# Kernel optimization log

Hardware: AMD Instinct MI355X
Metric: run time of the kernel (lower is better)

Reference implementation:

```python
import jax, jax.numpy as jnp
import numpy as np

D = 128      # d_feat / d_model
L = 512      # seq_len
H = 8        # heads (hardcoded in FourierBlock weights)
E = D // H   # head dim = 16
MODES = 64   # low-frequency modes (mode_select='low' -> index = range(MODES))
MA = 25      # moving_avg kernel
NL = 2       # e_layers
DFF = 512
EPS = 1e-5


def _positional(length, dim):
    pos = jnp.arange(length, dtype=jnp.float32)[:, None]
    div = jnp.exp(jnp.arange(0, dim, 2, dtype=jnp.float32) * (-np.log(10000.0) / dim))
    pe = jnp.zeros((length, dim), dtype=jnp.float32)
    pe = pe.at[:, 0::2].set(jnp.sin(pos * div))
    pe = pe.at[:, 1::2].set(jnp.cos(pos * div))
    return pe


def _mov_mean(x, k):
    # series_decomp moving average: replicate-pad (k-1)//2 each side, window mean stride 1
    pad = (k - 1) // 2
    xp = jnp.concatenate([jnp.repeat(x[:, :1], pad, axis=1), x,
                          jnp.repeat(x[:, -1:], pad, axis=1)], axis=1)
    cs = jnp.cumsum(xp, axis=1)
    cs = jnp.concatenate([jnp.zeros_like(cs[:, :1]), cs], axis=1)
    return (cs[:, k:] - cs[:, :-k]) / k


def _fourier_layer(x, Wq, bq, Wo, bo, fwr, fwi):
    # AutoCorrelationLayer(query proj -> FourierBlock -> out proj); k/v projections are unused by FourierBlock
    B = x.shape[0]
    q = (x @ Wq + bq).reshape(B, L, H, E).transpose(0, 2, 3, 1)   # B,H,E,L
    xft = jnp.fft.rfft(q, axis=-1)                                # B,H,E,L//2+1
    Wc = fwr + 1j * fwi                                           # H,E,E,M (complex mode weights)
    sel = jnp.einsum('bhem,heom->bhom', xft[..., :MODES], Wc)
    out_ft = jnp.zeros((B, H, E, L // 2 + 1), dtype=sel.dtype).at[..., :MODES].set(sel)
    y = jnp.fft.irfft(out_ft, n=L, axis=-1)                       # B,H,E,L
    y = y.reshape(B, L, H * E)  # matches torch .view(B, L, -1) on contiguous B,H,E,L
    return y @ Wo + bo


def _enc_layer(x, Wq, bq, Wo, bo, fwr, fwi, W1, W2):
    x = x + _fourier_layer(x, Wq, bq, Wo, bo, fwr, fwi)
    x = x - _mov_mean(x, MA)                                  # decomp1 seasonal part
    y = jax.nn.gelu(x @ W1, approximate=False) @ W2           # 1x1 convs == matmuls, no bias
    s = x + y
    return s - _mov_mean(s, MA)                               # decomp2 seasonal part


def setup_inputs() -> dict:
    key = jax.random.key(0)
    ks = jax.random.split(key, 12)
    B = 128
    scale = 1.0 / (D * D)
    return {
        "x_enc": jax.random.normal(ks[0], (B, D * L), dtype=jnp.float32),
        "x_mark_enc": jax.random.uniform(ks[1], (B, D * L), dtype=jnp.float32),
        "x_dec": jnp.zeros((1,), jnp.float32),
        "x_mark_dec": jnp.zeros((1,), jnp.float32),
        "conv_w": jax.random.normal(ks[2], (D, D, 3), dtype=jnp.float32) * 0.02,
        "Wq": jax.random.normal(ks[3], (NL, D, D), dtype=jnp.float32) * 0.02,
        "bq": jnp.zeros((NL, D), jnp.float32),
        "Wo": jax.random.normal(ks[4], (NL, D, D), dtype=jnp.float32) * 0.02,
        "bo": jnp.zeros((NL, D), jnp.float32),
        "fwr": jax.random.uniform(ks[5], (NL, H, E, E, MODES), dtype=jnp.float32) * scale,
        "fwi": jax.random.uniform(ks[6], (NL, H, E, E, MODES), dtype=jnp.float32) * scale,
        "W1": jax.random.normal(ks[7], (NL, D, DFF), dtype=jnp.float32) * 0.02,
        "W2": jax.random.normal(ks[8], (NL, DFF, D), dtype=jnp.float32) * 0.02,
        "ln_g": jnp.ones((D,), jnp.float32),
        "ln_b": jnp.zeros((D,), jnp.float32),
        "proj_w": jax.random.normal(ks[9], (D * L,), dtype=jnp.float32) * 0.002,
        "proj_b": jnp.zeros((), jnp.float32),
    }


def reference(x_enc, x_mark_enc, x_dec, x_mark_dec, conv_w, Wq, bq, Wo, bo,
              fwr, fwi, W1, W2, ln_g, ln_b, proj_w, proj_b):
    B = x_enc.shape[0]
    x = x_enc.reshape(B, D, L).transpose(0, 2, 1)          # B,L,D
    mark = x_mark_enc.reshape(B, D, L).transpose(0, 2, 1)  # B,L,D
    # TokenEmbedding: Conv1d kernel 3, circular padding, no bias
    xc = x.transpose(0, 2, 1)                              # B,D,L
    xp = jnp.concatenate([xc[:, :, -1:], xc, xc[:, :, :1]], axis=-1)
    tok = jax.lax.conv_general_dilated(xp, conv_w, (1,), 'VALID',
                                       dimension_numbers=('NCH', 'OIH', 'NCH'))
    h = tok.transpose(0, 2, 1) + _positional(L, D)[None]   # + sinusoidal PE (dropout=0)
    for l in range(NL):
        h = _enc_layer(h, Wq[l], bq[l], Wo[l], bo[l], fwr[l], fwi[l], W1[l], W2[l])
    # my_Layernorm: LayerNorm over features, then subtract mean over time axis
    mu = h.mean(-1, keepdims=True)
    var = h.var(-1, keepdims=True)
    hn = (h - mu) / jnp.sqrt(var + EPS) * ln_g + ln_b
    hn = hn - hn.mean(axis=1, keepdims=True)
    o = jax.nn.gelu(hn, approximate=False) * mark          # act + mask-mul
    return o.reshape(B, -1) @ proj_w + proj_b              # (B,) after squeeze
```

## Files before the change

### kernel.cpp

```cpp
#include <hip/hip_runtime.h>
#include <math.h>

#define DFF 512
#define NLAYER 2
#define TS_LD 132
#define CS_LD 130

typedef __bf16 bf16x8 __attribute__((ext_vector_type(8)));
typedef __bf16 bf16x4 __attribute__((ext_vector_type(4)));
typedef float f32x4 __attribute__((ext_vector_type(4)));

__device__ __forceinline__ float4 f4_load(const float* p) { return *(const float4*)p; }
__device__ __forceinline__ void f4_store(float* p, float4 v) { *(float4*)p = v; }
__device__ __forceinline__ float4 f4_zero() { return make_float4(0.f, 0.f, 0.f, 0.f); }
__device__ __forceinline__ float gelu_f(float x) {
    return 0.5f * x * (1.0f + erff(x * 0.70710678118654752440f));
}
__device__ __forceinline__ float gelu_fast(float x) {
    float z = 1.5957691216f * (x + 0.044715f * x * x * x);
    float e = __expf(z);
    return x - x / (e + 1.0f);
}
__device__ __forceinline__ void store_bf4(__bf16* p, float4 v) {
    __bf16 t[4] = {(__bf16)v.x, (__bf16)v.y, (__bf16)v.z, (__bf16)v.w};
    *(uint2*)p = *(uint2*)t;
}
__device__ __forceinline__ bf16x8 ld_b64x2(const __bf16* p) {
    bf16x4 lo = *(const bf16x4*)p;
    bf16x4 hi = *(const bf16x4*)(p + 4);
    return __builtin_shufflevector(lo, hi, 0, 1, 2, 3, 4, 5, 6, 7);
}

__global__ __launch_bounds__(256) void k_init(float* __restrict__ pe,
                                              __bf16* __restrict__ Fttb,
                                              __bf16* __restrict__ Gtb) {
    int idx = blockIdx.x * 256 + threadIdx.x;
    {
        int l = idx >> 7, d = idx & 127;
        int j = d >> 1;
        double div = exp((double)(2 * j) * (-log(10000.0) / 128.0));
        double a = (double)l * div;
        pe[idx] = (d & 1) ? (float)cos(a) : (float)sin(a);
    }
    {
        int m2 = idx >> 9, t = idx & 511;
        int m = m2 >> 1;
        int r = (m * t) & 511;
        double ang = (double)r * (6.283185307179586476925287 / 512.0);
        float cv = (float)cos(ang), sv = (float)sin(ang);
        float f = (m2 & 1) ? -sv : cv;
        Fttb[idx] = (__bf16)f;
        float s = (m == 0) ? (1.0f / 512.0f) : (2.0f / 512.0f);
        Gtb[t * 128 + m2] = (__bf16)(f * s);
    }
}

__global__ __launch_bounds__(256) void k_castw(const float* __restrict__ Wq,
                                               const float* __restrict__ Wo,
                                               const float* __restrict__ W1,
                                               const float* __restrict__ W2,
                                               const float* __restrict__ cw,
                                               __bf16* __restrict__ wbf,
                                               __bf16* __restrict__ cwtk) {
    int i = blockIdx.x * 256 + threadIdx.x;
    if (i < 65536) {
        int r = i & 16383, l = (i >> 14) & 1;
        int n = r >> 7, k = r & 127;
        const float* W = (i >= 32768) ? Wo : Wq;
        wbf[i] = (__bf16)W[l * 16384 + k * 128 + n];
    } else if (i < 196608) {
        int j = i - 65536;
        int l = j >> 16, r = j & 65535;
        int f = r >> 7, k = r & 127;
        wbf[i] = (__bf16)W1[l * 65536 + k * 512 + f];
    } else if (i < 327680) {
        int j = i - 196608;
        int l = j >> 16, r = j & 65535;
        int n = r >> 9, f = r & 511;
        wbf[i] = (__bf16)W2[l * 65536 + f * 128 + n];
    } else if (i < 376832) {
        int j = i - 327680;
        int s = j >> 14, r = j & 16383;
        int d = r >> 7, ii = r & 127;
        cwtk[j] = (__bf16)cw[(d * 128 + ii) * 3 + s];
    }
}

__global__ __launch_bounds__(256) void k_xpose(const float* __restrict__ xe,
                                               __bf16* __restrict__ xt) {
    __shared__ float ts[128][65];
    const int b = blockIdx.y, l0 = blockIdx.x * 64;
    for (int idx = threadIdx.x; idx < 128 * 16; idx += 256) {
        int d = idx >> 4, c4 = idx & 15;
        float4 v = f4_load(&xe[((size_t)b * 128 + d) * 512 + l0 + c4 * 4]);
        ts[d][c4 * 4 + 0] = v.x; ts[d][c4 * 4 + 1] = v.y;
        ts[d][c4 * 4 + 2] = v.z; ts[d][c4 * 4 + 3] = v.w;
    }
    __syncthreads();
#pragma unroll
    for (int p = 0; p < 4; ++p) {
        int l = (threadIdx.x >> 4) + p * 16;
        int d0 = (threadIdx.x & 15) * 8;
        __bf16 tmp[8];
#pragma unroll
        for (int j = 0; j < 8; ++j) tmp[j] = (__bf16)ts[d0 + j][l];
        *(uint4*)&xt[((size_t)b * 512 + l0 + l) * 128 + d0] = *(uint4*)tmp;
    }
}

__global__ __launch_bounds__(256, 4) void k_embed_m(const __bf16* __restrict__ xt,
                                                    const __bf16* __restrict__ cwtk,
                                                    const float* __restrict__ pe,
                                                    float* __restrict__ h,
                                                    __bf16* __restrict__ hb) {
    const int b = blockIdx.x >> 3, l0 = (blockIdx.x & 7) * 64;
    const int lane = threadIdx.x & 63, wid = threadIdx.x >> 6;
    const int wrow = (wid & 1) * 32, wcol = (wid >> 1) * 64;
    const int m16 = lane & 15, quad = lane >> 4;
    f32x4 acc[2][4];
#pragma unroll
    for (int a = 0; a < 2; ++a)
#pragma unroll
        for (int bb = 0; bb < 4; ++bb) acc[a][bb] = {0.f, 0.f, 0.f, 0.f};
#pragma unroll
    for (int s = 0; s < 3; ++s) {
#pragma unroll
        for (int ks = 0; ks < 4; ++ks) {
            const int ko = ks * 32 + quad * 8;
            bf16x8 af[2], bfr[4];
#pragma unroll
            for (int rt = 0; rt < 2; ++rt) {
                int gl = (l0 + wrow + rt * 16 + m16 + s - 1) & 511;
                af[rt] = *(const bf16x8*)&xt[(((size_t)b * 512 + gl) << 7) + ko];
            }
#pragma unroll
            for (int ct = 0; ct < 4; ++ct)
                bfr[ct] = *(const bf16x8*)&cwtk[((size_t)(s * 128 + wcol + ct * 16 + m16) << 7) + ko];
#pragma unroll
            for (int rt = 0; rt < 2; ++rt)
#pragma unroll
                for (int ct = 0; ct < 4; ++ct)
                    acc[rt][ct] = __builtin_amdgcn_mfma_f32_16x16x32_bf16(
                        af[rt], bfr[ct], acc[rt][ct], 0, 0, 0);
        }
    }
#pragma unroll
    for (int ct = 0; ct < 4; ++ct) {
        int gcol = wcol + ct * 16 + m16;
#pragma unroll
        for (int rt = 0; rt < 2; ++rt)
#pragma unroll
            for (int r = 0; r < 4; ++r) {
                int l = l0 + wrow + rt * 16 + quad * 4 + r;
                float v = acc[rt][ct][r] + pe[l * 128 + gcol];
                size_t gi = (((size_t)b * 512 + l) << 7) + gcol;
                h[gi] = v;
                hb[gi] = (__bf16)v;
            }
    }
}

__global__ __launch_bounds__(256, 4) void k_qprojT(const __bf16* __restrict__ Xb,
                                                   const __bf16* __restrict__ Wt,
                                                   const float* __restrict__ bias,
                                                   __bf16* __restrict__ qT) {
    const int rowBase = blockIdx.x * 64;
    const int lane = threadIdx.x & 63, wid = threadIdx.x >> 6;
    const int wn = (wid & 1) * 64, wr = (wid >> 1) * 32;
    const int m16 = lane & 15, quad = lane >> 4;
    f32x4 acc[4][2];
#pragma unroll
    for (int a = 0; a < 4; ++a)
#pragma unroll
        for (int b = 0; b < 2; ++b) acc[a][b] = {0.f, 0.f, 0.f, 0.f};
#pragma unroll
    for (int ks = 0; ks < 4; ++ks) {
        const int ko = ks * 32 + quad * 8;
        bf16x8 wf[4], xf[2];
#pragma unroll
        for (int rt = 0; rt < 4; ++rt)
            wf[rt] = *(const bf16x8*)&Wt[((size_t)(wn + rt * 16 + m16) << 7) + ko];
#pragma unroll
        for (int ct = 0; ct < 2; ++ct)
            xf[ct] = *(const bf16x8*)&Xb[((size_t)(rowBase + wr + ct * 16 + m16) << 7) + ko];
#pragma unroll
        for (int rt = 0; rt < 4; ++rt)
#pragma unroll
            for (int ct = 0; ct < 2; ++ct)
                acc[rt][ct] = __builtin_amdgcn_mfma_f32_16x16x32_bf16(
                    wf[rt], xf[ct], acc[rt][ct], 0, 0, 0);
    }
#pragma unroll
    for (int rt = 0; rt < 4; ++rt)
#pragma unroll
        for (int r = 0; r < 4; ++r) {
            int n = wn + rt * 16 + quad * 4 + r;
            float bv = bias[n];
#pragma unroll
            for (int ct = 0; ct < 2; ++ct) {
                int grow = rowBase + wr + ct * 16 + m16;
                qT[(size_t)n * 65536 + grow] = (__bf16)(acc[rt][ct][r] + bv);
            }
        }
}

__global__ __launch_bounds__(128) void k_fdftmix(const __bf16* __restrict__ qT,
                                                 const __bf16* __restrict__ Fttb,
                                                 const float* __restrict__ fwr,
                                                 const float* __restrict__ fwi,
                                                 __bf16* __restrict__ ddb) {
    __shared__ float cs[32][CS_LD];
    const int b = blockIdx.y, d0 = blockIdx.x * 32;
    const int lane = threadIdx.x & 63, wid = threadIdx.x >> 6;
    const int wm = wid * 64;
    const int m16 = lane & 15, quad = lane >> 4;
    f32x4 acc[2][4];
#pragma unroll
    for (int a = 0; a < 2; ++a)
#pragma unroll
        for (int bb = 0; bb < 4; ++bb) acc[a][bb] = {0.f, 0.f, 0.f, 0.f};
    for (int ks = 0; ks < 16; ++ks) {
        const int ko = ks * 32 + quad * 8;
        bf16x8 af[2], bf[4];
#pragma unroll
        for (int rt = 0; rt < 2; ++rt)
            af[rt] = *(const bf16x8*)&qT[(size_t)(d0 + rt * 16 + m16) * 65536 + b * 512 + ko];
#pragma unroll
        for (int ct = 0; ct < 4; ++ct)
            bf[ct] = *(const bf16x8*)&Fttb[(size_t)(wm + ct * 16 + m16) * 512 + ko];
#pragma unroll
        for (int rt = 0; rt < 2; ++rt)
#pragma unroll
            for (int ct = 0; ct < 4; ++ct)
                acc[rt][ct] = __builtin_amdgcn_mfma_f32_16x16x32_bf16(
                    af[rt], bf[ct], acc[rt][ct], 0, 0, 0);
    }
#pragma unroll
    for (int rt = 0; rt < 2; ++rt)
#pragma unroll
        for (int ct = 0; ct < 4; ++ct)
#pragma unroll
            for (int r = 0; r < 4; ++r)
                cs[rt * 16 + quad * 4 + r][wm + ct * 16 + m16] = acc[rt][ct][r];
    __syncthreads();
    const int m = threadIdx.x & 63, og = threadIdx.x >> 6;
#pragma unroll
    for (int lh = 0; lh < 2; ++lh) {
        int hh = (d0 >> 4) + lh;
#pragma unroll
        for (int oi = 0; oi < 8; ++oi) {
            int o = og * 8 + oi;
            float dr = 0.f, di = 0.f;
#pragma unroll
            for (int e = 0; e < 16; ++e) {
                float2 cv = *(const float2*)&cs[lh * 16 + e][2 * m];
                float wr = fwr[(((size_t)hh * 16 + e) * 16 + o) * 64 + m];
                float wi = fwi[(((size_t)hh * 16 + e) * 16 + o) * 64 + m];
                dr += cv.x * wr - cv.y * wi;
                di += cv.x * wi + cv.y * wr;
            }
            __bf16 t2[2] = {(__bf16)dr, (__bf16)di};
            *(uint*)&ddb[((size_t)b * 128 + hh * 16 + o) * 128 + 2 * m] = *(uint*)t2;
        }
    }
}

__global__ __launch_bounds__(256, 4) void k_idft_m(const __bf16* __restrict__ ddb,
                                                   const __bf16* __restrict__ Gtb,
                                                   __bf16* __restrict__ y) {
    const int b = blockIdx.y;
    const int t0 = (blockIdx.x & 3) * 128, hob = (blockIdx.x >> 2) * 64;
    const int lane = threadIdx.x & 63, wid = threadIdx.x >> 6;
    const int wt = (wid & 1) * 64, wh = (wid >> 1) * 32;
    const int m16 = lane & 15, quad = lane >> 4;
    f32x4 acc[4][2];
#pragma unroll
    for (int a = 0; a < 4; ++a)
#pragma unroll
        for (int bb = 0; bb < 2; ++bb) acc[a][bb] = {0.f, 0.f, 0.f, 0.f};
#pragma unroll
    for (int ks = 0; ks < 4; ++ks) {
        const int ko = ks * 32 + quad * 8;
        bf16x8 af[4], bf[2];
#pragma unroll
        for (int rt = 0; rt < 4; ++rt)
            af[rt] = *(const bf16x8*)&Gtb[(size_t)(t0 + wt + rt * 16 + m16) * 128 + ko];
#pragma unroll
        for (int ct = 0; ct < 2; ++ct)
            bf[ct] = *(const bf16x8*)&ddb[((size_t)b * 128 + hob + wh + ct * 16 + m16) * 128 + ko];
#pragma unroll
        for (int rt = 0; rt < 4; ++rt)
#pragma unroll
            for (int ct = 0; ct < 2; ++ct)
                acc[rt][ct] = __builtin_amdgcn_mfma_f32_16x16x32_bf16(
                    af[rt], bf[ct], acc[rt][ct], 0, 0, 0);
    }
#pragma unroll
    for (int rt = 0; rt < 4; ++rt)
#pragma unroll
        for (int ct = 0; ct < 2; ++ct) {
            int ho = hob + wh + ct * 16 + m16;
            int tb = t0 + wt + rt * 16 + quad * 4;
            __bf16 tmp[4] = {(__bf16)acc[rt][ct][0], (__bf16)acc[rt][ct][1],
                             (__bf16)acc[rt][ct][2], (__bf16)acc[rt][ct][3]};
            *(uint2*)&y[((size_t)b * 128 + ho) * 512 + tb] = *(uint2*)tmp;
        }
}

template <bool RES>
__global__ __launch_bounds__(256, 4) void k_mgemm(const __bf16* __restrict__ Xb,
                                                  const __bf16* __restrict__ Wt,
                                                  const float* __restrict__ bias,
                                                  const float* __restrict__ R,
                                                  float* __restrict__ out) {
    const int rowBase = blockIdx.x * 64;
    const int lane = threadIdx.x & 63, wid = threadIdx.x >> 6;
    const int wrow = (wid & 1) * 32, wcol = (wid >> 1) * 64;
    const int m16 = lane & 15, quad = lane >> 4;
    f32x4 acc[2][4];
#pragma unroll
    for (int a = 0; a < 2; ++a)
#pragma unroll
        for (int b = 0; b < 4; ++b) acc[a][b] = {0.f, 0.f, 0.f, 0.f};
#pragma unroll
    for (int ks = 0; ks < 4; ++ks) {
        const int ko = ks * 32 + quad * 8;
        bf16x8 af[2], bfr[4];
#pragma unroll
        for (int rt = 0; rt < 2; ++rt)
            af[rt] = *(const bf16x8*)&Xb[((size_t)(rowBase + wrow + rt * 16 + m16) << 7) + ko];
#pragma unroll
        for (int ct = 0; ct < 4; ++ct)
            bfr[ct] = *(const bf16x8*)&Wt[((size_t)(wcol + ct * 16 + m16) << 7) + ko];
#pragma unroll
        for (int rt = 0; rt < 2; ++rt)
#pragma unroll
            for (int ct = 0; ct < 4; ++ct)
                acc[rt][ct] = __builtin_amdgcn_mfma_f32_16x16x32_bf16(
                    af[rt], bfr[ct], acc[rt][ct], 0, 0, 0);
    }
#pragma unroll
    for (int ct = 0; ct < 4; ++ct) {
        int gcol = wcol + ct * 16 + m16;
        float bv = bias[gcol];
#pragma unroll
        for (int rt = 0; rt < 2; ++rt)
#pragma unroll
            for (int r = 0; r < 4; ++r) {
                size_t gi = ((size_t)(rowBase + wrow + rt * 16 + quad * 4 + r) << 7) + gcol;
                float v = acc[rt][ct][r] + bv;
                if (RES) v += R[gi];
                out[gi] = v;
            }
    }
}

__global__ __launch_bounds__(256, 4) void k_ffnm(const __bf16* __restrict__ Xb,
                                                 const float* __restrict__ Xf,
                                                 const __bf16* __restrict__ W1t,
                                                 const __bf16* __restrict__ W2t,
                                                 float* __restrict__ out) {
    __shared__ __align__(16) __bf16 ts[64 * TS_LD];
    const int rowBase = blockIdx.x * 64;
    const int lane = threadIdx.x & 63, wid = threadIdx.x >> 6;
    const int wrow = (wid & 1) * 32, wcol = (wid >> 1) * 64;
    const int m16 = lane & 15, quad = lane >> 4;
    f32x4 acc2[2][4];
#pragma unroll
    for (int a = 0; a < 2; ++a)
#pragma unroll
        for (int b = 0; b < 4; ++b) acc2[a][b] = {0.f, 0.f, 0.f, 0.f};

    for (int f0 = 0; f0 < DFF; f0 += 128) {
        f32x4 c1[2][4];
#pragma unroll
        for (int a = 0; a < 2; ++a)
#pragma unroll
            for (int b = 0; b < 4; ++b) c1[a][b] = {0.f, 0.f, 0.f, 0.f};
#pragma unroll
        for (int ks = 0; ks < 4; ++ks) {
            const int ko = ks * 32 + quad * 8;
            bf16x8 af[2], bfr[4];
#pragma unroll
            for (int rt = 0; rt < 2; ++rt)
                af[rt] = *(const bf16x8*)&Xb[((size_t)(rowBase + wrow + rt * 16 + m16) << 7) + ko];
#pragma unroll
            for (int ct = 0; ct < 4; ++ct)
                bfr[ct] = *(const bf16x8*)&W1t[((size_t)(f0 + wcol + ct * 16 + m16) << 7) + ko];
#pragma unroll
            for (int rt = 0; rt < 2; ++rt)
#pragma unroll
                for (int ct = 0; ct < 4; ++ct)
                    c1[rt][ct] = __builtin_amdgcn_mfma_f32_16x16x32_bf16(
                        af[rt], bfr[ct], c1[rt][ct], 0, 0, 0);
        }
#pragma unroll
        for (int rt = 0; rt < 2; ++rt)
#pragma unroll
            for (int ct = 0; ct < 4; ++ct)
#pragma unroll
                for (int r = 0; r < 4; ++r) {
                    int lrow = wrow + rt * 16 + quad * 4 + r;
                    int lcol = wcol + ct * 16 + m16;
                    ts[lrow * TS_LD + lcol] = (__bf16)gelu_fast(c1[rt][ct][r]);
                }
        __syncthreads();
#pragma unroll
        for (int ks = 0; ks < 4; ++ks) {
            const int ko = ks * 32 + quad * 8;
            bf16x8 af[2], bfr[4];
#pragma unroll
            for (int rt = 0; rt < 2; ++rt)
                af[rt] = ld_b64x2(&ts[(wrow + rt * 16 + m16) * TS_LD + ko]);
#pragma unroll
            for (int ct = 0; ct < 4; ++ct)
                bfr[ct] = *(const bf16x8*)&W2t[((size_t)(wcol + ct * 16 + m16) << 9) + f0 + ko];
#pragma unroll
            for (int rt = 0; rt < 2; ++rt)
#pragma unroll
                for (int ct = 0; ct < 4; ++ct)
                    acc2[rt][ct] = __builtin_amdgcn_mfma_f32_16x16x32_bf16(
                        af[rt], bfr[ct], acc2[rt][ct], 0, 0, 0);
        }
        __syncthreads();
    }
#pragma unroll
    for (int ct = 0; ct < 4; ++ct) {
        int gcol = wcol + ct * 16 + m16;
#pragma unroll
        for (int rt = 0; rt < 2; ++rt)
#pragma unroll
            for (int r = 0; r < 4; ++r) {
                size_t gi = ((size_t)(rowBase + wrow + rt * 16 + quad * 4 + r) << 7) + gcol;
                out[gi] = acc2[rt][ct][r] + Xf[gi];
            }
    }
}

__global__ __launch_bounds__(256) void k_decomp(const float* __restrict__ X,
                                                float* __restrict__ out,
                                                __bf16* __restrict__ outb) {
    __shared__ float xs[152][64];
    const int b = blockIdx.y;
    const int l0 = (blockIdx.x >> 1) * 128, dh = (blockIdx.x & 1) * 64;
    for (int idx = threadIdx.x; idx < 152 * 16; idx += 256) {
        int r = idx >> 4, c4 = idx & 15;
        int gl = l0 - 12 + r;
        gl = gl < 0 ? 0 : (gl > 511 ? 511 : gl);
        f4_store(&xs[r][c4 * 4],
                 f4_load(&X[((size_t)b * 512 + gl) * 128 + dh + c4 * 4]));
    }
    __syncthreads();
    const int dg = threadIdx.x & 15, lg = threadIdx.x >> 4;
    const int d0 = dg * 4, base = lg * 8;
    float4 s = f4_zero();
#pragma unroll
    for (int w = 0; w < 25; ++w) {
        float4 v = f4_load(&xs[base + w][d0]);
        s.x += v.x; s.y += v.y; s.z += v.z; s.w += v.w;
    }
    const float inv = 1.0f / 25.0f;
#pragma unroll
    for (int i = 0; i < 8; ++i) {
        int t = base + 12 + i;
        float4 x = f4_load(&xs[t][d0]);
        float4 o = make_float4(x.x - s.x * inv, x.y - s.y * inv,
                               x.z - s.z * inv, x.w - s.w * inv);
        size_t gi = ((size_t)b * 512 + l0 + lg * 8 + i) * 128 + dh + d0;
        f4_store(&out[gi], o);
        store_bf4(&outb[gi], o);
        if (i < 7) {
            float4 a = f4_load(&xs[base + 25 + i][d0]);
            float4 r = f4_load(&xs[base + i][d0]);
            s.x += a.x - r.x; s.y += a.y - r.y; s.z += a.z - r.z; s.w += a.w - r.w;
        }
    }
}

__global__ __launch_bounds__(256) void k_ln(const float* __restrict__ X,
                                            const float* __restrict__ g,
                                            const float* __restrict__ bb,
                                            float* __restrict__ out) {
    const int row = blockIdx.x * 4 + (threadIdx.x >> 6);
    const int lane = threadIdx.x & 63;
    float2 v = *(const float2*)&X[(size_t)row * 128 + lane * 2];
    float s = v.x + v.y, ss = v.x * v.x + v.y * v.y;
#pragma unroll
    for (int o = 32; o; o >>= 1) {
        s += __shfl_xor(s, o);
        ss += __shfl_xor(ss, o);
    }
    float mu = s * (1.0f / 128.0f);
    float var = ss * (1.0f / 128.0f) - mu * mu;
    float rstd = rsqrtf(var + 1e-5f);
    float2 gg = *(const float2*)&g[lane * 2];
    float2 bv = *(const float2*)&bb[lane * 2];
    float2 o;
    o.x = (v.x - mu) * rstd * gg.x + bv.x;
    o.y = (v.y - mu) * rstd * gg.y + bv.y;
    *(float2*)&out[(size_t)row * 128 + lane * 2] = o;
}

__global__ __launch_bounds__(128) void k_colmean(const float* __restrict__ X,
                                                 float* __restrict__ cm) {
    const int b = blockIdx.y, l0 = blockIdx.x * 64, d = threadIdx.x;
    float s = 0.f;
    for (int l = l0; l < l0 + 64; ++l) s += X[((size_t)b * 512 + l) * 128 + d];
    atomicAdd(&cm[b * 128 + d], s);
}

__global__ __launch_bounds__(128) void k_final(const float* __restrict__ hn,
                                               const float* __restrict__ cm,
                                               const float* __restrict__ mark,
                                               const float* __restrict__ pw,
                                               const float* __restrict__ pb,
                                               float* __restrict__ out) {
    const int b = blockIdx.y, l0 = blockIdx.x * 128, d = threadIdx.x;
    const float c = cm[b * 128 + d] * (1.0f / 512.0f);
    float acc = 0.f;
    for (int l = l0; l < l0 + 128; ++l) {
        float v = hn[((size_t)b * 512 + l) * 128 + d] - c;
        acc += gelu_f(v) * mark[((size_t)b * 128 + d) * 512 + l] * pw[l * 128 + d];
    }
    __shared__ float red[2];
#pragma unroll
    for (int o = 32; o; o >>= 1) acc += __shfl_xor(acc, o);
    if ((threadIdx.x & 63) == 0) red[threadIdx.x >> 6] = acc;
    __syncthreads();
    if (threadIdx.x == 0) {
        float tot = red[0] + red[1];
        if (blockIdx.x == 0) tot += pb[0];
        atomicAdd(&out[b], tot);
    }
}

extern "C" void kernel_launch(void* const* d_in, const int* in_sizes, int n_in,
                              void* d_out, int out_size, void* d_ws, size_t ws_size,
                              hipStream_t stream) {
    const float* xe   = (const float*)d_in[0];
    const float* mark = (const float*)d_in[1];
    const float* cw   = (const float*)d_in[4];
    const float* Wq   = (const float*)d_in[5];
    const float* bq   = (const float*)d_in[6];
    const float* Wo   = (const float*)d_in[7];
    const float* bo   = (const float*)d_in[8];
    const float* fwr  = (const float*)d_in[9];
    const float* fwi  = (const float*)d_in[10];
    const float* W1   = (const float*)d_in[11];
    const float* W2   = (const float*)d_in[12];
    const float* lng  = (const float*)d_in[13];
    const float* lnb  = (const float*)d_in[14];
    const float* pw   = (const float*)d_in[15];
    const float* pb   = (const float*)d_in[16];
    float* out = (float*)d_out;

    float* ws    = (float*)d_ws;
    __bf16* Fttb = (__bf16*)ws;
    __bf16* Gtb  = (__bf16*)(ws + 65536);
    float* h     = ws + 131072;
    float* bufA  = ws + 8519680;
    __bf16* hb   = (__bf16*)(ws + 16908288);
    float* yrg   = ws + 21102592;
    float* cm    = ws + 25296896;
    __bf16* wbf  = (__bf16*)(ws + 25313280);
    float* pe    = yrg;
    __bf16* cwtk = (__bf16*)(yrg + 65536);
    __bf16* yb   = (__bf16*)yrg;
    __bf16* xt   = (__bf16*)bufA;
    __bf16* qT   = (__bf16*)bufA;
    __bf16* ddb  = (__bf16*)(bufA + 4194304);
    __bf16* Wqt  = wbf;
    __bf16* Wot  = wbf + 32768;
    __bf16* W1t  = wbf + 65536;
    __bf16* W2t  = wbf + 196608;

    k_init<<<256, 256, 0, stream>>>(pe, Fttb, Gtb);
    k_castw<<<1472, 256, 0, stream>>>(Wq, Wo, W1, W2, cw, wbf, cwtk);
    k_xpose<<<dim3(8, 128), 256, 0, stream>>>(xe, xt);
    k_embed_m<<<1024, 256, 0, stream>>>(xt, cwtk, pe, h, hb);
    for (int l = 0; l < NLAYER; ++l) {
        k_qprojT<<<1024, 256, 0, stream>>>(hb, Wqt + l * 16384, bq + l * 128, qT);
        k_fdftmix<<<dim3(4, 128), 128, 0, stream>>>(qT, Fttb, fwr + l * 131072,
                                                    fwi + l * 131072, ddb);
        k_idft_m<<<dim3(8, 128), 256, 0, stream>>>(ddb, Gtb, yb);
        k_mgemm<true><<<1024, 256, 0, stream>>>(yb, Wot + l * 16384, bo + l * 128,
                                                h, bufA);
        k_decomp<<<dim3(8, 128), 256, 0, stream>>>(bufA, h, hb);
        k_ffnm<<<1024, 256, 0, stream>>>(hb, h, W1t + l * 65536, W2t + l * 65536, bufA);
        k_decomp<<<dim3(8, 128), 256, 0, stream>>>(bufA, h, hb);
    }
    k_ln<<<16384, 256, 0, stream>>>(h, lng, lnb, bufA);
    hipMemsetAsync(cm, 0, 16384 * sizeof(float), stream);
    k_colmean<<<dim3(8, 128), 128, 0, stream>>>(bufA, cm);
    hipMemsetAsync(d_out, 0, 128 * sizeof(float), stream);
    k_final<<<dim3(4, 128), 128, 0, stream>>>(bufA, cm, mark, pw, pb, out);

    (void)in_sizes; (void)n_in; (void)out_size; (void)ws_size;
}
```

Before: 719.7 us.

## Fuse series decomposition into out-projection and FFN GEMM epilogues with halo recompute

The out-projection GEMM and the FFN kernel now each compute a 96-row tile (64 output rows plus 16-row halos on each side) and stage the residual-added result in shared memory. The 25-tap moving-average subtraction then runs in the epilogue, so the separate decomp kernels and their full-tensor global round trips are removed. The cost is 50% redundant GEMM work for the halo rows, a larger shared-memory footprint with lower occupancy (launch bounds 3), and a second bf16 buffer so input and output no longer alias.

Result: faster. 675.4 us (-6.2%).

```diff
diff --git a/kernel.cpp b/kernel.cpp
--- a/kernel.cpp
+++ b/kernel.cpp
@@ -3,8 +3,9 @@
 
 #define DFF 512
 #define NLAYER 2
-#define TS_LD 132
 #define CS_LD 130
+#define SS_LD 130
+#define TS2_LD 68
 
 typedef __bf16 bf16x8 __attribute__((ext_vector_type(8)));
 typedef __bf16 bf16x4 __attribute__((ext_vector_type(4)));
@@ -30,6 +31,7 @@
     bf16x4 hi = *(const bf16x4*)(p + 4);
     return __builtin_shufflevector(lo, hi, 0, 1, 2, 3, 4, 5, 6, 7);
 }
+__device__ __forceinline__ int clampl(int v) { return v < 0 ? 0 : (v > 511 ? 511 : v); }
 
 __global__ __launch_bounds__(256) void k_init(float* __restrict__ pe,
                                               __bf16* __restrict__ Fttb,
@@ -307,33 +309,36 @@
         }
 }
 
-template <bool RES>
-__global__ __launch_bounds__(256, 4) void k_mgemm(const __bf16* __restrict__ Xb,
-                                                  const __bf16* __restrict__ Wt,
-                                                  const float* __restrict__ bias,
-                                                  const float* __restrict__ R,
-                                                  float* __restrict__ out) {
-    const int rowBase = blockIdx.x * 64;
+__global__ __launch_bounds__(256, 3) void k_mgd(const __bf16* __restrict__ yb,
+                                                const __bf16* __restrict__ Wt,
+                                                const float* __restrict__ bias,
+                                                const float* __restrict__ hres,
+                                                float* __restrict__ outf,
+                                                __bf16* __restrict__ outb) {
+    __shared__ float ss[96 * SS_LD];
+    const int b = blockIdx.x >> 3, l0 = (blockIdx.x & 7) * 64;
     const int lane = threadIdx.x & 63, wid = threadIdx.x >> 6;
-    const int wrow = (wid & 1) * 32, wcol = (wid >> 1) * 64;
+    const int wrow = (wid & 1) * 48, wcol = (wid >> 1) * 64;
     const int m16 = lane & 15, quad = lane >> 4;
-    f32x4 acc[2][4];
-#pragma unroll
-    for (int a = 0; a < 2; ++a)
-#pragma unroll
-        for (int b = 0; b < 4; ++b) acc[a][b] = {0.f, 0.f, 0.f, 0.f};
+    f32x4 acc[3][4];
+#pragma unroll
+    for (int a = 0; a < 3; ++a)
+#pragma unroll
+        for (int bb = 0; bb < 4; ++bb) acc[a][bb] = {0.f, 0.f, 0.f, 0.f};
 #pragma unroll
     for (int ks = 0; ks < 4; ++ks) {
         const int ko = ks * 32 + quad * 8;
-        bf16x8 af[2], bfr[4];
-#pragma unroll
-        for (int rt = 0; rt < 2; ++rt)
-            af[rt] = *(const bf16x8*)&Xb[((size_t)(rowBase + wrow + rt * 16 + m16) << 7) + ko];
+        bf16x8 af[3], bfr[4];
+#pragma unroll
+        for (int rt = 0; rt < 3; ++rt) {
+            int gl = clampl(l0 - 16 + wrow + rt * 16 + m16);
+            af[rt] = *(const bf16x8*)&yb[(((size_t)b * 512 + gl) << 7) + ko];
+        }
 #pragma unroll
         for (int ct = 0; ct < 4; ++ct)
             bfr[ct] = *(const bf16x8*)&Wt[((size_t)(wcol + ct * 16 + m16) << 7) + ko];
 #pragma unroll
-        for (int rt = 0; rt < 2; ++rt)
+        for (int rt = 0; rt < 3; ++rt)
 #pragma unroll
             for (int ct = 0; ct < 4; ++ct)
                 acc[rt][ct] = __builtin_amdgcn_mfma_f32_16x16x32_bf16(
@@ -341,82 +346,113 @@
     }
 #pragma unroll
     for (int ct = 0; ct < 4; ++ct) {
-        int gcol = wcol + ct * 16 + m16;
-        float bv = bias[gcol];
-#pragma unroll
-        for (int rt = 0; rt < 2; ++rt)
+        int col = wcol + ct * 16 + m16;
+        float bv = bias[col];
+#pragma unroll
+        for (int rt = 0; rt < 3; ++rt)
 #pragma unroll
             for (int r = 0; r < 4; ++r) {
-                size_t gi = ((size_t)(rowBase + wrow + rt * 16 + quad * 4 + r) << 7) + gcol;
-                float v = acc[rt][ct][r] + bv;
-                if (RES) v += R[gi];
-                out[gi] = v;
+                int row = wrow + rt * 16 + quad * 4 + r;
+                int gl = clampl(l0 - 16 + row);
+                ss[row * SS_LD + col] =
+                    acc[rt][ct][r] + bv + hres[(((size_t)b * 512 + gl) << 7) + col];
             }
     }
-}
-
-__global__ __launch_bounds__(256, 4) void k_ffnm(const __bf16* __restrict__ Xb,
-                                                 const float* __restrict__ Xf,
-                                                 const __bf16* __restrict__ W1t,
-                                                 const __bf16* __restrict__ W2t,
-                                                 float* __restrict__ out) {
-    __shared__ __align__(16) __bf16 ts[64 * TS_LD];
-    const int rowBase = blockIdx.x * 64;
+    __syncthreads();
+    const int dg = threadIdx.x & 31, lg = threadIdx.x >> 5;
+    const int d0 = dg * 4, base = lg * 8;
+    float4 s = f4_zero();
+#pragma unroll
+    for (int w = 0; w < 25; ++w) {
+        float4 v = f4_load(&ss[(base + 4 + w) * SS_LD + d0]);
+        s.x += v.x; s.y += v.y; s.z += v.z; s.w += v.w;
+    }
+    const float inv = 1.0f / 25.0f;
+#pragma unroll
+    for (int i = 0; i < 8; ++i) {
+        float4 x = f4_load(&ss[(base + 16 + i) * SS_LD + d0]);
+        float4 o = make_float4(x.x - s.x * inv, x.y - s.y * inv,
+                               x.z - s.z * inv, x.w - s.w * inv);
+        size_t gi = (((size_t)b * 512 + l0 + base + i) << 7) + d0;
+        f4_store(&outf[gi], o);
+        store_bf4(&outb[gi], o);
+        if (i < 7) {
+            float4 a = f4_load(&ss[(base + 29 + i) * SS_LD + d0]);
+            float4 r = f4_load(&ss[(base + 4 + i) * SS_LD + d0]);
+            s.x += a.x - r.x; s.y += a.y - r.y; s.z += a.z - r.z; s.w += a.w - r.w;
+        }
+    }
+}
+
+__global__ __launch_bounds__(256, 3) void k_ffd(const __bf16* __restrict__ Xb,
+                                                const float* __restrict__ Xf,
+                                                const __bf16* __restrict__ W1t,
+                                                const __bf16* __restrict__ W2t,
+                                                float* __restrict__ outf,
+                                                __bf16* __restrict__ outb) {
+    __shared__ __align__(16) float ss[96 * SS_LD];
+    __bf16* ts = (__bf16*)ss;
+    const int b = blockIdx.x >> 3, l0 = (blockIdx.x & 7) * 64;
     const int lane = threadIdx.x & 63, wid = threadIdx.x >> 6;
-    const int wrow = (wid & 1) * 32, wcol = (wid >> 1) * 64;
+    const int wrow = (wid & 1) * 48;
+    const int wcolF = (wid >> 1) * 32;
+    const int wcolO = (wid >> 1) * 64;
     const int m16 = lane & 15, quad = lane >> 4;
-    f32x4 acc2[2][4];
-#pragma unroll
-    for (int a = 0; a < 2; ++a)
-#pragma unroll
-        for (int b = 0; b < 4; ++b) acc2[a][b] = {0.f, 0.f, 0.f, 0.f};
-
-    for (int f0 = 0; f0 < DFF; f0 += 128) {
-        f32x4 c1[2][4];
-#pragma unroll
-        for (int a = 0; a < 2; ++a)
-#pragma unroll
-            for (int b = 0; b < 4; ++b) c1[a][b] = {0.f, 0.f, 0.f, 0.f};
+    f32x4 acc2[3][4];
+#pragma unroll
+    for (int a = 0; a < 3; ++a)
+#pragma unroll
+        for (int bb = 0; bb < 4; ++bb) acc2[a][bb] = {0.f, 0.f, 0.f, 0.f};
+
+    for (int fc = 0; fc < 8; ++fc) {
+        const int f0 = fc * 64;
+        f32x4 c1[3][2];
+#pragma unroll
+        for (int a = 0; a < 3; ++a)
+#pragma unroll
+            for (int bb = 0; bb < 2; ++bb) c1[a][bb] = {0.f, 0.f, 0.f, 0.f};
 #pragma unroll
         for (int ks = 0; ks < 4; ++ks) {
             const int ko = ks * 32 + quad * 8;
-            bf16x8 af[2], bfr[4];
-#pragma unroll
-            for (int rt = 0; rt < 2; ++rt)
-                af[rt] = *(const bf16x8*)&Xb[((size_t)(rowBase + wrow + rt * 16 + m16) << 7) + ko];
-#pragma unroll
-            for (int ct = 0; ct < 4; ++ct)
-                bfr[ct] = *(const bf16x8*)&W1t[((size_t)(f0 + wcol + ct * 16 + m16) << 7) + ko];
-#pragma unroll
-            for (int rt = 0; rt < 2; ++rt)
-#pragma unroll
-                for (int ct = 0; ct < 4; ++ct)
+            bf16x8 af[3], bfr[2];
+#pragma unroll
+            for (int rt = 0; rt < 3; ++rt) {
+                int gl = clampl(l0 - 16 + wrow + rt * 16 + m16);
+                af[rt] = *(const bf16x8*)&Xb[(((size_t)b * 512 + gl) << 7) + ko];
+            }
+#pragma unroll
+            for (int ct = 0; ct < 2; ++ct)
+                bfr[ct] = *(const bf16x8*)&W1t[((size_t)(f0 + wcolF + ct * 16 + m16) << 7) + ko];
+#pragma unroll
+            for (int rt = 0; rt < 3; ++rt)
+#pragma unroll
+                for (int ct = 0; ct < 2; ++ct)
                     c1[rt][ct] = __builtin_amdgcn_mfma_f32_16x16x32_bf16(
                         af[rt], bfr[ct], c1[rt][ct], 0, 0, 0);
         }
 #pragma unroll
-        for (int rt = 0; rt < 2; ++rt)
-#pragma unroll
-            for (int ct = 0; ct < 4; ++ct)
+        for (int rt = 0; rt < 3; ++rt)
+#pragma unroll
+            for (int ct = 0; ct < 2; ++ct)
 #pragma unroll
                 for (int r = 0; r < 4; ++r) {
                     int lrow = wrow + rt * 16 + quad * 4 + r;
-                    int lcol = wcol + ct * 16 + m16;
-                    ts[lrow * TS_LD + lcol] = (__bf16)gelu_fast(c1[rt][ct][r]);
+                    int lcol = wcolF + ct * 16 + m16;
+                    ts[lrow * TS2_LD + lcol] = (__bf16)gelu_fast(c1[rt][ct][r]);
                 }
         __syncthreads();
 #pragma unroll
-        for (int ks = 0; ks < 4; ++ks) {
-            const int ko = ks * 32 + quad * 8;
-            bf16x8 af[2], bfr[4];
-#pragma unroll
-            for (int rt = 0; rt < 2; ++rt)
-                af[rt] = ld_b64x2(&ts[(wrow + rt * 16 + m16) * TS_LD + ko]);
+        for (int ks2 = 0; ks2 < 2; ++ks2) {
+            const int ko2 = ks2 * 32 + quad * 8;
+            bf16x8 af[3], bfr[4];
+#pragma unroll
+            for (int rt = 0; rt < 3; ++rt)
+                af[rt] = ld_b64x2(&ts[(wrow + rt * 16 + m16) * TS2_LD + ko2]);
 #pragma unroll
             for (int ct = 0; ct < 4; ++ct)
-                bfr[ct] = *(const bf16x8*)&W2t[((size_t)(wcol + ct * 16 + m16) << 9) + f0 + ko];
-#pragma unroll
-            for (int rt = 0; rt < 2; ++rt)
+                bfr[ct] = *(const bf16x8*)&W2t[((size_t)(wcolO + ct * 16 + m16) << 9) + f0 + ko2];
+#pragma unroll
+            for (int rt = 0; rt < 3; ++rt)
 #pragma unroll
                 for (int ct = 0; ct < 4; ++ct)
                     acc2[rt][ct] = __builtin_amdgcn_mfma_f32_16x16x32_bf16(
@@ -426,52 +462,38 @@
     }
 #pragma unroll
     for (int ct = 0; ct < 4; ++ct) {
-        int gcol = wcol + ct * 16 + m16;
-#pragma unroll
-        for (int rt = 0; rt < 2; ++rt)
+        int col = wcolO + ct * 16 + m16;
+#pragma unroll
+        for (int rt = 0; rt < 3; ++rt)
 #pragma unroll
             for (int r = 0; r < 4; ++r) {
-                size_t gi = ((size_t)(rowBase + wrow + rt * 16 + quad * 4 + r) << 7) + gcol;
-                out[gi] = acc2[rt][ct][r] + Xf[gi];
+                int row = wrow + rt * 16 + quad * 4 + r;
+                int gl = clampl(l0 - 16 + row);
+                ss[row * SS_LD + col] =
+                    acc2[rt][ct][r] + Xf[(((size_t)b * 512 + gl) << 7) + col];
             }
     }
-}
-
-__global__ __launch_bounds__(256) void k_decomp(const float* __restrict__ X,
-                                                float* __restrict__ out,
-                                                __bf16* __restrict__ outb) {
-    __shared__ float xs[152][64];
-    const int b = blockIdx.y;
-    const int l0 = (blockIdx.x >> 1) * 128, dh = (blockIdx.x & 1) * 64;
-    for (int idx = threadIdx.x; idx < 152 * 16; idx += 256) {
-        int r = idx >> 4, c4 = idx & 15;
-        int gl = l0 - 12 + r;
-        gl = gl < 0 ? 0 : (gl > 511 ? 511 : gl);
-        f4_store(&xs[r][c4 * 4],
-                 f4_load(&X[((size_t)b * 512 + gl) * 128 + dh + c4 * 4]));
-    }
     __syncthreads();
-    const int dg = threadIdx.x & 15, lg = threadIdx.x >> 4;
+    const int dg = threadIdx.x & 31, lg = threadIdx.x >> 5;
     const int d0 = dg * 4, base = lg * 8;
     float4 s = f4_zero();
 #pragma unroll
     for (int w = 0; w < 25; ++w) {
-        float4 v = f4_load(&xs[base + w][d0]);
+        float4 v = f4_load(&ss[(base + 4 + w) * SS_LD + d0]);
         s.x += v.x; s.y += v.y; s.z += v.z; s.w += v.w;
     }
     const float inv = 1.0f / 25.0f;
 #pragma unroll
     for (int i = 0; i < 8; ++i) {
-        int t = base + 12 + i;
-        float4 x = f4_load(&xs[t][d0]);
+        float4 x = f4_load(&ss[(base + 16 + i) * SS_LD + d0]);
         float4 o = make_float4(x.x - s.x * inv, x.y - s.y * inv,
                                x.z - s.z * inv, x.w - s.w * inv);
-        size_t gi = ((size_t)b * 512 + l0 + lg * 8 + i) * 128 + dh + d0;
-        f4_store(&out[gi], o);
+        size_t gi = (((size_t)b * 512 + l0 + base + i) << 7) + d0;
+        f4_store(&outf[gi], o);
         store_bf4(&outb[gi], o);
         if (i < 7) {
-            float4 a = f4_load(&xs[base + 25 + i][d0]);
-            float4 r = f4_load(&xs[base + i][d0]);
+            float4 a = f4_load(&ss[(base + 29 + i) * SS_LD + d0]);
+            float4 r = f4_load(&ss[(base + 4 + i) * SS_LD + d0]);
             s.x += a.x - r.x; s.y += a.y - r.y; s.z += a.z - r.z; s.w += a.w - r.w;
         }
     }
@@ -559,10 +581,11 @@
     __bf16* Gtb  = (__bf16*)(ws + 65536);
     float* h     = ws + 131072;
     float* bufA  = ws + 8519680;
-    __bf16* hb   = (__bf16*)(ws + 16908288);
-    float* yrg   = ws + 21102592;
-    float* cm    = ws + 25296896;
-    __bf16* wbf  = (__bf16*)(ws + 25313280);
+    __bf16* hb0  = (__bf16*)(ws + 16908288);
+    __bf16* hb1  = (__bf16*)(ws + 21102592);
+    float* yrg   = ws + 25296896;
+    float* cm    = ws + 29491200;
+    __bf16* wbf  = (__bf16*)(ws + 29507584);
     float* pe    = yrg;
     __bf16* cwtk = (__bf16*)(yrg + 65536);
     __bf16* yb   = (__bf16*)yrg;
@@ -577,17 +600,16 @@
     k_init<<<256, 256, 0, stream>>>(pe, Fttb, Gtb);
     k_castw<<<1472, 256, 0, stream>>>(Wq, Wo, W1, W2, cw, wbf, cwtk);
     k_xpose<<<dim3(8, 128), 256, 0, stream>>>(xe, xt);
-    k_embed_m<<<1024, 256, 0, stream>>>(xt, cwtk, pe, h, hb);
+    k_embed_m<<<1024, 256, 0, stream>>>(xt, cwtk, pe, h, hb0);
     for (int l = 0; l < NLAYER; ++l) {
-        k_qprojT<<<1024, 256, 0, stream>>>(hb, Wqt + l * 16384, bq + l * 128, qT);
+        k_qprojT<<<1024, 256, 0, stream>>>(hb0, Wqt + l * 16384, bq + l * 128, qT);
         k_fdftmix<<<dim3(4, 128), 128, 0, stream>>>(qT, Fttb, fwr + l * 131072,
                                                     fwi + l * 131072, ddb);
         k_idft_m<<<dim3(8, 128), 256, 0, stream>>>(ddb, Gtb, yb);
-        k_mgemm<true><<<1024, 256, 0, stream>>>(yb, Wot + l * 16384, bo + l * 128,
-                                                h, bufA);
-        k_decomp<<<dim3(8, 128), 256, 0, stream>>>(bufA, h, hb);
-        k_ffnm<<<1024, 256, 0, stream>>>(hb, h, W1t + l * 65536, W2t + l * 65536, bufA);
-        k_decomp<<<dim3(8, 128), 256, 0, stream>>>(bufA, h, hb);
+        k_mgd<<<1024, 256, 0, stream>>>(yb, Wot + l * 16384, bo + l * 128,
+                                        h, bufA, hb1);
+        k_ffd<<<1024, 256, 0, stream>>>(hb1, bufA, W1t + l * 65536,
+                                        W2t + l * 65536, h, hb0);
     }
     k_ln<<<16384, 256, 0, stream>>>(h, lng, lnb, bufA);
     hipMemsetAsync(cm, 0, 16384 * sizeof(float), stream);
```
